# Kernel optimization log

Hardware: AMD Instinct MI355X
Metric: run time of the kernel (lower is better)

Reference implementation:

```python
import jax, jax.numpy as jnp
import numpy as np

N = 100000        # nodes
E = 1600000       # edges (avg degree 16)
D_IN = 128        # input_dim
HID = 128         # hidden
L = 2             # num_layers
EPS = 1e-5        # LayerNorm eps (torch default)


def setup_inputs() -> dict:
    key = jax.random.key(0)
    ks = jax.random.split(key, 5)
    x = jax.random.normal(ks[0], (N, D_IN), dtype=jnp.float32)
    edge_index = jax.random.randint(ks[1], (2, E), 0, N, dtype=jnp.int64)
    e_feat = jax.random.uniform(ks[2], (E,), dtype=jnp.float32)
    # nn.Linear(input_dim, hidden): weight [hidden, input_dim], bias [hidden]
    lin_w = jax.random.normal(ks[3], (HID, D_IN), dtype=jnp.float32) / np.float32(np.sqrt(D_IN))
    lin_b = jax.random.normal(ks[4], (HID,), dtype=jnp.float32) * 0.01
    ln_scale = jnp.ones((L, HID), dtype=jnp.float32)
    ln_bias = jnp.zeros((L, HID), dtype=jnp.float32)
    return {"x": x, "edge_index": edge_index, "e_feat": e_feat,
            "lin_w": lin_w, "lin_b": lin_b,
            "ln_scale": ln_scale, "ln_bias": ln_bias}


def _layernorm(h, scale, bias):
    mu = jnp.mean(h, axis=-1, keepdims=True)
    var = jnp.mean(jnp.square(h - mu), axis=-1, keepdims=True)
    return (h - mu) * jax.lax.rsqrt(var + EPS) * scale + bias


def reference(x, edge_index, e_feat, lin_w, lin_b, ln_scale, ln_bias):
    src, dst = edge_index[0], edge_index[1]
    h = x @ lin_w.T + lin_b            # [N, HID]
    ori = h
    for i in range(L):
        if i != 0:                      # res=True
            h = h + ori
        h = _layernorm(h, ln_scale[i], ln_bias[i])   # norm=True
        h = jax.nn.relu(h)              # relu=True; dp=0 -> dropout no-op
        # GraphConv(weight=False, bias=False): weighted SpMM aggregation
        msg = h[src] * e_feat[:, None]  # [E, HID]
        h = jax.ops.segment_sum(msg, dst, num_segments=N)  # [N, HID]
    return h
```

## Files before the change

### kernel.cpp

```cpp
#include <hip/hip_runtime.h>


constexpr int N_NODES = 100000;
constexpr int N_EDGES = 1600000;
constexpr int HID     = 128;
constexpr int NBKT    = (N_NODES + 511) / 512;
constexpr int BCAP    = 9216;
constexpr float LN_EPS = 1e-5f;

typedef __attribute__((ext_vector_type(8))) short short8;
typedef __attribute__((ext_vector_type(4))) float floatx4;

__device__ inline unsigned pack_bf16x2(float a, float b) {
    unsigned ua = __float_as_uint(a), ub = __float_as_uint(b);
    ua += 0x7fff + ((ua >> 16) & 1);
    ub += 0x7fff + ((ub >> 16) & 1);
    return (ua >> 16) | (ub & 0xffff0000u);
}
__device__ inline float bflo(unsigned u) { return __uint_as_float(u << 16); }
__device__ inline float bfhi(unsigned u) { return __uint_as_float(u & 0xffff0000u); }

__global__ __launch_bounds__(256) void k_bin(const int* __restrict__ ei,
                                             const float* __restrict__ ef,
                                             int* __restrict__ gcur,
                                             int* __restrict__ gbufDst,
                                             int2* __restrict__ gbufSW) {
    __shared__ int cnt[NBKT];
    __shared__ int incl[256];
    __shared__ int gbase[NBKT];
    __shared__ int sdst[2048];
    __shared__ int2 ssw[2048];
    const int t = threadIdx.x;

    for (int e0 = blockIdx.x * 2048; e0 < N_EDGES; e0 += gridDim.x * 2048) {
        for (int i = t; i < NBKT; i += 256) cnt[i] = 0;
        __syncthreads();

        const int nE = min(2048, N_EDGES - e0);
        int ed[8], es[8], ep[8]; float ew[8];
        const int base = e0 + t * 8;
        if (base + 8 <= N_EDGES) {
            int4 s0 = *(const int4*)&ei[base];
            int4 s1 = *(const int4*)&ei[base + 4];
            int4 d0 = *(const int4*)&ei[N_EDGES + base];
            int4 d1 = *(const int4*)&ei[N_EDGES + base + 4];
            float4 w0 = *(const float4*)&ef[base];
            float4 w1 = *(const float4*)&ef[base + 4];
            es[0]=s0.x; es[1]=s0.y; es[2]=s0.z; es[3]=s0.w;
            es[4]=s1.x; es[5]=s1.y; es[6]=s1.z; es[7]=s1.w;
            ed[0]=d0.x; ed[1]=d0.y; ed[2]=d0.z; ed[3]=d0.w;
            ed[4]=d1.x; ed[5]=d1.y; ed[6]=d1.z; ed[7]=d1.w;
            ew[0]=w0.x; ew[1]=w0.y; ew[2]=w0.z; ew[3]=w0.w;
            ew[4]=w1.x; ew[5]=w1.y; ew[6]=w1.z; ew[7]=w1.w;
#pragma unroll
            for (int k = 0; k < 8; ++k) ep[k] = atomicAdd(&cnt[ed[k] >> 9], 1);
        } else {
#pragma unroll
            for (int k = 0; k < 8; ++k) {
                int idx = base + k;
                if (idx < N_EDGES) {
                    es[k] = ei[idx]; ed[k] = ei[N_EDGES + idx]; ew[k] = ef[idx];
                    ep[k] = atomicAdd(&cnt[ed[k] >> 9], 1);
                } else ed[k] = -1;
            }
        }
        __syncthreads();

        int v = (t < NBKT) ? cnt[t] : 0;
        incl[t] = v;
        for (int o = 1; o < 256; o <<= 1) {
            __syncthreads();
            int u = (t >= o) ? incl[t - o] : 0;
            __syncthreads();
            incl[t] += u;
        }
        __syncthreads();
        if (t < NBKT) gbase[t] = atomicAdd(&gcur[t], v);
        __syncthreads();

#pragma unroll
        for (int k = 0; k < 8; ++k) {
            if (ed[k] < 0) continue;
            int b = ed[k] >> 9;
            int idx = incl[b] - cnt[b] + ep[k];
            sdst[idx] = ed[k];
            ssw[idx] = make_int2(es[k], __float_as_int(ew[k]));
        }
        __syncthreads();

        for (int j = t; j < nE; j += 256) {
            int d = sdst[j];
            int b = d >> 9;
            int pos = gbase[b] + (j - (incl[b] - cnt[b]));
            if (pos < BCAP) {
                gbufDst[(size_t)b * BCAP + pos] = d;
                gbufSW [(size_t)b * BCAP + pos] = ssw[j];
            }
        }
        __syncthreads();
    }
}

__global__ __launch_bounds__(512) void k_build(const int* __restrict__ gcur,
                                               const int* __restrict__ gbufDst,
                                               const int2* __restrict__ gbufSW,
                                               int* __restrict__ rp,
                                               int2* __restrict__ csr) {
    __shared__ int cnt[512];
    __shared__ int cur[512];
    __shared__ int2 sorted[BCAP];
    const int t     = threadIdx.x;
    const int b     = blockIdx.x;
    const int nbase = b * 512;

    int v0 = (t < NBKT) ? min(gcur[t], BCAP) : 0;
    cnt[t] = v0;
    for (int o = 1; o < 512; o <<= 1) {
        __syncthreads();
        int u = (t >= o) ? cnt[t - o] : 0;
        __syncthreads();
        cnt[t] += u;
    }
    __syncthreads();
    const int nb = min(gcur[b], BCAP);
    const int cb = cnt[b] - nb;
    if (b == NBKT - 1 && t == 0) rp[N_NODES] = cnt[NBKT - 1];
    __syncthreads();

    const int*  bd = gbufDst + (size_t)b * BCAP;
    const int2* bs = gbufSW  + (size_t)b * BCAP;

    cnt[t] = 0;
    __syncthreads();
    for (int i = t; i < nb; i += 512) atomicAdd(&cnt[bd[i] - nbase], 1);
    __syncthreads();

    int v = cnt[t];
    for (int o = 1; o < 512; o <<= 1) {
        __syncthreads();
        int u = (t >= o) ? cnt[t - o] : 0;
        __syncthreads();
        cnt[t] += u;
    }
    __syncthreads();
    const int excl = cnt[t] - v;
    cur[t] = excl;
    if (nbase + t < N_NODES) rp[nbase + t] = cb + excl;
    __syncthreads();

    for (int i = t; i < nb; i += 512) {
        int d = bd[i];
        int pos = atomicAdd(&cur[d - nbase], 1);
        sorted[pos] = bs[i];
    }
    __syncthreads();
    for (int i = t; i < nb; i += 512) csr[(size_t)cb + i] = sorted[i];
}

__global__ __launch_bounds__(256) void k_gemm_mfma(const float* __restrict__ x,
                                                   const float* __restrict__ W,
                                                   const float* __restrict__ bias,
                                                   const float* __restrict__ lns,
                                                   const float* __restrict__ lnb,
                                                   unsigned* __restrict__ orib,
                                                   unsigned* __restrict__ hact) {
    __shared__ __align__(16) char smem[128 * 136 * 2 + 64 * 136 * 2];
    ushort (*Ws)[136] = (ushort(*)[136])smem;
    ushort (*Xs)[136] = (ushort(*)[136])(smem + 128 * 136 * 2);
    float  (*Hs)[132] = (float(*)[132])smem;

    const int t    = threadIdx.x;
    const int row0 = blockIdx.x * 64;

    {
        const float4* Wf = (const float4*)W;
#pragma unroll
        for (int i = 0; i < 8; ++i) {
            int g = t + 256 * i;
            float4 p = Wf[g * 2], q = Wf[g * 2 + 1];
            uint4 vv = make_uint4(pack_bf16x2(p.x, p.y), pack_bf16x2(p.z, p.w),
                                  pack_bf16x2(q.x, q.y), pack_bf16x2(q.z, q.w));
            int r = g >> 4;
            int c = (g & 15) * 8;
            *(uint4*)&Ws[r][c] = vv;
        }
    }
    {
        const float4* xg = (const float4*)x;
        const int base = blockIdx.x * 2048;
#pragma unroll
        for (int i = 0; i < 8; ++i) {
            int f = t + 256 * i;
            int g = base + f;
            float4 vv = make_float4(0.f, 0.f, 0.f, 0.f);
            if (g < N_NODES * 32) vv = xg[g];
            int r = f >> 5;
            int c = (f & 31) * 4;
            uint2 p = make_uint2(pack_bf16x2(vv.x, vv.y), pack_bf16x2(vv.z, vv.w));
            *(uint2*)&Xs[r][c] = p;
        }
    }
    __syncthreads();

    const int wv   = t >> 6;
    const int l    = t & 63;
    const int mrow = l & 15;
    const int kq   = l >> 4;

    floatx4 acc[8];
#pragma unroll
    for (int i = 0; i < 8; ++i) acc[i] = (floatx4){0.f, 0.f, 0.f, 0.f};

#pragma unroll
    for (int ks = 0; ks < 4; ++ks) {
        short8 a = *(const short8*)&Xs[wv * 16 + mrow][ks * 32 + kq * 8];
#pragma unroll
        for (int tc = 0; tc < 8; ++tc) {
            short8 bb = *(const short8*)&Ws[tc * 16 + mrow][ks * 32 + kq * 8];
            acc[tc] = __builtin_amdgcn_mfma_f32_16x16x32_bf16(a, bb, acc[tc], 0, 0, 0);
        }
    }
    __syncthreads();

#pragma unroll
    for (int tc = 0; tc < 8; ++tc)
#pragma unroll
        for (int r = 0; r < 4; ++r)
            Hs[wv * 16 + kq * 4 + r][tc * 16 + mrow] = acc[tc][r];
    __syncthreads();

    const float2 b2  = ((const float2*)bias)[l];
    const float2 sc2 = ((const float2*)lns)[l];
    const float2 bb2 = ((const float2*)lnb)[l];
    for (int rr = 0; rr < 16; ++rr) {
        const int lrow = wv * 16 + rr;
        const int grow = row0 + lrow;
        if (grow >= N_NODES) break;
        float2 vv = *(const float2*)&Hs[lrow][l * 2];
        vv.x += b2.x; vv.y += b2.y;
        orib[(size_t)grow * 64 + l] = pack_bf16x2(vv.x, vv.y);
        float s  = vv.x + vv.y;
        float s2 = vv.x * vv.x + vv.y * vv.y;
#pragma unroll
        for (int m = 1; m < 64; m <<= 1) {
            s  += __shfl_xor(s, m);
            s2 += __shfl_xor(s2, m);
        }
        const float mu   = s * (1.0f / 128.0f);
        const float var  = s2 * (1.0f / 128.0f) - mu * mu;
        const float rstd = rsqrtf(var + LN_EPS);
        float y0 = fmaxf((vv.x - mu) * rstd * sc2.x + bb2.x, 0.0f);
        float y1 = fmaxf((vv.y - mu) * rstd * sc2.y + bb2.y, 0.0f);
        hact[(size_t)grow * 64 + l] = pack_bf16x2(y0, y1);
    }
}

__device__ inline void spmm_body(const int* __restrict__ rp,
                                 const int2* __restrict__ csr,
                                 const uint2* __restrict__ H2,
                                 int n, int l32, int deg, int beg, int maxd,
                                 float& a0, float& a1, float& a2, float& a3) {
    for (int j = 0; j < maxd; j += 4) {
#pragma unroll
        for (int k = 0; k < 4; ++k) {
            const int jj = j + k;
            const bool valid = jj < deg;
            const int idx = valid ? beg + jj : 0;
            int2 c = csr[idx];
            float w = valid ? __int_as_float(c.y) : 0.0f;
            uint2 v = H2[(size_t)c.x * 32 + l32];
            a0 += w * bflo(v.x);
            a1 += w * bfhi(v.x);
            a2 += w * bflo(v.y);
            a3 += w * bfhi(v.y);
        }
    }
}

__global__ __launch_bounds__(256) void k_spmm_ln(const int* __restrict__ rp,
                                                 const int2* __restrict__ csr,
                                                 const unsigned* __restrict__ Hb,
                                                 const unsigned* __restrict__ orib,
                                                 const float* __restrict__ lns,
                                                 const float* __restrict__ lnb,
                                                 unsigned* __restrict__ hout) {
    const int wid  = (blockIdx.x * 256 + threadIdx.x) >> 6;
    const int lane = threadIdx.x & 63;
    const int half = lane >> 5;
    const int l32  = lane & 31;
    const int n    = wid * 2 + half;

    const int beg = rp[n];
    const int deg = rp[n + 1] - beg;
    int maxd = deg;
    maxd = max(maxd, __shfl_xor(maxd, 32));

    float a0 = 0.f, a1 = 0.f, a2 = 0.f, a3 = 0.f;
    spmm_body(rp, csr, (const uint2*)Hb, n, l32, deg, beg, maxd, a0, a1, a2, a3);

    uint2 o = ((const uint2*)orib)[(size_t)n * 32 + l32];
    float v0 = a0 + bflo(o.x), v1 = a1 + bfhi(o.x);
    float v2 = a2 + bflo(o.y), v3 = a3 + bfhi(o.y);
    float s  = v0 + v1 + v2 + v3;
    float s2 = v0 * v0 + v1 * v1 + v2 * v2 + v3 * v3;
#pragma unroll
    for (int m = 1; m < 32; m <<= 1) {
        s  += __shfl_xor(s, m);
        s2 += __shfl_xor(s2, m);
    }
    const float mu   = s * (1.0f / 128.0f);
    const float var  = s2 * (1.0f / 128.0f) - mu * mu;
    const float rstd = rsqrtf(var + LN_EPS);
    const float4 sc = ((const float4*)lns)[l32];
    const float4 bb = ((const float4*)lnb)[l32];
    float y0 = fmaxf((v0 - mu) * rstd * sc.x + bb.x, 0.0f);
    float y1 = fmaxf((v1 - mu) * rstd * sc.y + bb.y, 0.0f);
    float y2 = fmaxf((v2 - mu) * rstd * sc.z + bb.z, 0.0f);
    float y3 = fmaxf((v3 - mu) * rstd * sc.w + bb.w, 0.0f);
    ((uint2*)hout)[(size_t)n * 32 + l32] =
        make_uint2(pack_bf16x2(y0, y1), pack_bf16x2(y2, y3));
}

__global__ __launch_bounds__(256) void k_spmm_out(const int* __restrict__ rp,
                                                  const int2* __restrict__ csr,
                                                  const unsigned* __restrict__ Hb,
                                                  float* __restrict__ out) {
    const int wid  = (blockIdx.x * 256 + threadIdx.x) >> 6;
    const int lane = threadIdx.x & 63;
    const int half = lane >> 5;
    const int l32  = lane & 31;
    const int n    = wid * 2 + half;

    const int beg = rp[n];
    const int deg = rp[n + 1] - beg;
    int maxd = deg;
    maxd = max(maxd, __shfl_xor(maxd, 32));

    float a0 = 0.f, a1 = 0.f, a2 = 0.f, a3 = 0.f;
    spmm_body(rp, csr, (const uint2*)Hb, n, l32, deg, beg, maxd, a0, a1, a2, a3);

    ((float4*)out)[(size_t)n * 32 + l32] = make_float4(a0, a1, a2, a3);
}

extern "C" void kernel_launch(void* const* d_in, const int* in_sizes, int n_in,
                              void* d_out, int out_size, void* d_ws, size_t ws_size,
                              hipStream_t stream) {
    const float* x   = (const float*)d_in[0];
    const int*   ei  = (const int*)d_in[1];
    const float* ef  = (const float*)d_in[2];
    const float* W   = (const float*)d_in[3];
    const float* b   = (const float*)d_in[4];
    const float* lns = (const float*)d_in[5];
    const float* lnb = (const float*)d_in[6];
    float* out = (float*)d_out;

    unsigned* orib = (unsigned*)d_out;

    unsigned* hact  = (unsigned*)d_ws;
    unsigned* hact2 = hact + (size_t)N_NODES * 64;
    int2* csr    = (int2*)(hact2 + (size_t)N_NODES * 64);
    int2* gbufSW = csr + N_EDGES;
    int* gcur    = (int*)(gbufSW + (size_t)NBKT * BCAP);
    int* rp      = gcur + NBKT;
    int* gbufDst = rp + (N_NODES + 1);

    const int sb = N_NODES / 2 * 64 / 256;

    hipMemsetAsync(gcur, 0, NBKT * sizeof(int), stream);
    k_bin<<<256, 256, 0, stream>>>(ei, ef, gcur, gbufDst, gbufSW);
    k_build<<<NBKT, 512, 0, stream>>>(gcur, gbufDst, gbufSW, rp, csr);

    k_gemm_mfma<<<(N_NODES + 63) / 64, 256, 0, stream>>>(x, W, b, lns, lnb, orib, hact);

    k_spmm_ln<<<sb, 256, 0, stream>>>(rp, csr, hact, orib, lns + HID, lnb + HID, hact2);
    k_spmm_out<<<sb, 256, 0, stream>>>(rp, csr, hact2, out);
}
```

Before: 353.3 us.

## Map one wavefront per node in SpMM with uniform edge loops

Measured after the change: 311.3 us. -11.9%, faster.

```diff
diff --git a/kernel.cpp b/kernel.cpp
--- a/kernel.cpp
+++ b/kernel.cpp
@@ -255,25 +255,32 @@
     }
 }
 
-__device__ inline void spmm_body(const int* __restrict__ rp,
-                                 const int2* __restrict__ csr,
-                                 const uint2* __restrict__ H2,
-                                 int n, int l32, int deg, int beg, int maxd,
-                                 float& a0, float& a1, float& a2, float& a3) {
-    for (int j = 0; j < maxd; j += 4) {
-#pragma unroll
-        for (int k = 0; k < 4; ++k) {
-            const int jj = j + k;
-            const bool valid = jj < deg;
-            const int idx = valid ? beg + jj : 0;
-            int2 c = csr[idx];
-            float w = valid ? __int_as_float(c.y) : 0.0f;
-            uint2 v = H2[(size_t)c.x * 32 + l32];
-            a0 += w * bflo(v.x);
-            a1 += w * bfhi(v.x);
-            a2 += w * bflo(v.y);
-            a3 += w * bfhi(v.y);
-        }
+#define SPMM_ACC(cc)                                                      \
+    {                                                                     \
+        unsigned v = Hb[(size_t)(cc).x * 64 + lane];                      \
+        float w = __int_as_float((cc).y);                                 \
+        accx += w * bflo(v);                                              \
+        accy += w * bfhi(v);                                              \
+    }
+
+__device__ inline void spmm_row(const int2* __restrict__ csr,
+                                const unsigned* __restrict__ Hb,
+                                int beg, int end, int lane,
+                                float& accx, float& accy) {
+    int e = beg;
+    for (; e + 8 <= end; e += 8) {
+        int2 c0 = csr[e],     c1 = csr[e + 1], c2 = csr[e + 2], c3 = csr[e + 3];
+        int2 c4 = csr[e + 4], c5 = csr[e + 5], c6 = csr[e + 6], c7 = csr[e + 7];
+        SPMM_ACC(c0) SPMM_ACC(c1) SPMM_ACC(c2) SPMM_ACC(c3)
+        SPMM_ACC(c4) SPMM_ACC(c5) SPMM_ACC(c6) SPMM_ACC(c7)
+    }
+    for (; e + 2 <= end; e += 2) {
+        int2 c0 = csr[e], c1 = csr[e + 1];
+        SPMM_ACC(c0) SPMM_ACC(c1)
+    }
+    if (e < end) {
+        int2 c0 = csr[e];
+        SPMM_ACC(c0)
     }
 }
 
@@ -286,39 +293,30 @@
                                                  unsigned* __restrict__ hout) {
     const int wid  = (blockIdx.x * 256 + threadIdx.x) >> 6;
     const int lane = threadIdx.x & 63;
-    const int half = lane >> 5;
-    const int l32  = lane & 31;
-    const int n    = wid * 2 + half;
-
-    const int beg = rp[n];
-    const int deg = rp[n + 1] - beg;
-    int maxd = deg;
-    maxd = max(maxd, __shfl_xor(maxd, 32));
-
-    float a0 = 0.f, a1 = 0.f, a2 = 0.f, a3 = 0.f;
-    spmm_body(rp, csr, (const uint2*)Hb, n, l32, deg, beg, maxd, a0, a1, a2, a3);
-
-    uint2 o = ((const uint2*)orib)[(size_t)n * 32 + l32];
-    float v0 = a0 + bflo(o.x), v1 = a1 + bfhi(o.x);
-    float v2 = a2 + bflo(o.y), v3 = a3 + bfhi(o.y);
-    float s  = v0 + v1 + v2 + v3;
-    float s2 = v0 * v0 + v1 * v1 + v2 * v2 + v3 * v3;
-#pragma unroll
-    for (int m = 1; m < 32; m <<= 1) {
+
+    const int beg = __builtin_amdgcn_readfirstlane(rp[wid]);
+    const int end = __builtin_amdgcn_readfirstlane(rp[wid + 1]);
+
+    float accx = 0.f, accy = 0.f;
+    spmm_row(csr, Hb, beg, end, lane, accx, accy);
+
+    unsigned o = orib[(size_t)wid * 64 + lane];
+    float vx = accx + bflo(o), vy = accy + bfhi(o);
+    float s  = vx + vy;
+    float s2 = vx * vx + vy * vy;
+#pragma unroll
+    for (int m = 1; m < 64; m <<= 1) {
         s  += __shfl_xor(s, m);
         s2 += __shfl_xor(s2, m);
     }
     const float mu   = s * (1.0f / 128.0f);
     const float var  = s2 * (1.0f / 128.0f) - mu * mu;
     const float rstd = rsqrtf(var + LN_EPS);
-    const float4 sc = ((const float4*)lns)[l32];
-    const float4 bb = ((const float4*)lnb)[l32];
-    float y0 = fmaxf((v0 - mu) * rstd * sc.x + bb.x, 0.0f);
-    float y1 = fmaxf((v1 - mu) * rstd * sc.y + bb.y, 0.0f);
-    float y2 = fmaxf((v2 - mu) * rstd * sc.z + bb.z, 0.0f);
-    float y3 = fmaxf((v3 - mu) * rstd * sc.w + bb.w, 0.0f);
-    ((uint2*)hout)[(size_t)n * 32 + l32] =
-        make_uint2(pack_bf16x2(y0, y1), pack_bf16x2(y2, y3));
+    const float2 sc = ((const float2*)lns)[lane];
+    const float2 bb = ((const float2*)lnb)[lane];
+    float y0 = fmaxf((vx - mu) * rstd * sc.x + bb.x, 0.0f);
+    float y1 = fmaxf((vy - mu) * rstd * sc.y + bb.y, 0.0f);
+    hout[(size_t)wid * 64 + lane] = pack_bf16x2(y0, y1);
 }
 
 __global__ __launch_bounds__(256) void k_spmm_out(const int* __restrict__ rp,
@@ -327,19 +325,14 @@
                                                   float* __restrict__ out) {
     const int wid  = (blockIdx.x * 256 + threadIdx.x) >> 6;
     const int lane = threadIdx.x & 63;
-    const int half = lane >> 5;
-    const int l32  = lane & 31;
-    const int n    = wid * 2 + half;
-
-    const int beg = rp[n];
-    const int deg = rp[n + 1] - beg;
-    int maxd = deg;
-    maxd = max(maxd, __shfl_xor(maxd, 32));
-
-    float a0 = 0.f, a1 = 0.f, a2 = 0.f, a3 = 0.f;
-    spmm_body(rp, csr, (const uint2*)Hb, n, l32, deg, beg, maxd, a0, a1, a2, a3);
-
-    ((float4*)out)[(size_t)n * 32 + l32] = make_float4(a0, a1, a2, a3);
+
+    const int beg = __builtin_amdgcn_readfirstlane(rp[wid]);
+    const int end = __builtin_amdgcn_readfirstlane(rp[wid + 1]);
+
+    float accx = 0.f, accy = 0.f;
+    spmm_row(csr, Hb, beg, end, lane, accx, accy);
+
+    ((float2*)out)[(size_t)wid * 64 + lane] = make_float2(accx, accy);
 }
 
 extern "C" void kernel_launch(void* const* d_in, const int* in_sizes, int n_in,
@@ -364,7 +357,7 @@
     int* rp      = gcur + NBKT;
     int* gbufDst = rp + (N_NODES + 1);
 
-    const int sb = N_NODES / 2 * 64 / 256;
+    const int wb = N_NODES * 64 / 256;
 
     hipMemsetAsync(gcur, 0, NBKT * sizeof(int), stream);
     k_bin<<<256, 256, 0, stream>>>(ei, ef, gcur, gbufDst, gbufSW);
@@ -372,6 +365,6 @@
 
     k_gemm_mfma<<<(N_NODES + 63) / 64, 256, 0, stream>>>(x, W, b, lns, lnb, orib, hact);
 
-    k_spmm_ln<<<sb, 256, 0, stream>>>(rp, csr, hact, orib, lns + HID, lnb + HID, hact2);
-    k_spmm_out<<<sb, 256, 0, stream>>>(rp, csr, hact2, out);
-}
+    k_spmm_ln<<<wb, 256, 0, stream>>>(rp, csr, hact, orib, lns + HID, lnb + HID, hact2);
+    k_spmm_out<<<wb, 256, 0, stream>>>(rp, csr, hact2, out);
+}
```
